# Kernel optimization log

Hardware: AMD Instinct MI355X
Metric: run time of the kernel (lower is better)

## Reference

```python
import jax, jax.numpy as jnp
import numpy as np

NUM_GRAPHS = 512  # number of segments (graphs) in the batch
N_NODES = 200000
HIDDEN = 256


def setup_inputs() -> dict:
    key = jax.random.key(0)
    ks = jax.random.split(key, 8)
    x = jax.random.normal(ks[0], (N_NODES, HIDDEN), dtype=jnp.float32)
    batch = jnp.sort(jax.random.randint(ks[1], (N_NODES,), 0, NUM_GRAPHS, dtype=jnp.int32))
    h4 = HIDDEN // 4
    w1 = jax.random.normal(ks[2], (HIDDEN, h4), dtype=jnp.float32) * (1.0 / np.sqrt(HIDDEN))
    b1 = jnp.zeros((h4,), dtype=jnp.float32)
    w2 = jax.random.normal(ks[3], (h4, 1), dtype=jnp.float32) * (1.0 / np.sqrt(h4))
    b2 = jnp.zeros((1,), dtype=jnp.float32)
    wp = jax.random.normal(ks[4], (3 * HIDDEN, HIDDEN), dtype=jnp.float32) * (1.0 / np.sqrt(3 * HIDDEN))
    bp = jnp.zeros((HIDDEN,), dtype=jnp.float32)
    gamma = jnp.ones((HIDDEN,), dtype=jnp.float32)
    beta = jnp.zeros((HIDDEN,), dtype=jnp.float32)
    return {"x": x, "batch": batch, "w1": w1, "b1": b1, "w2": w2, "b2": b2,
            "wp": wp, "bp": bp, "gamma": gamma, "beta": beta}


def reference(x, batch, w1, b1, w2, b2, wp, bp, gamma, beta):
    G = NUM_GRAPHS
    # --- global mean pool ---
    seg_sum = jax.ops.segment_sum(x, batch, num_segments=G)  # [G, H]
    counts = jax.ops.segment_sum(jnp.ones((x.shape[0],), x.dtype), batch, num_segments=G)
    z_mean = seg_sum / jnp.maximum(counts, 1.0)[:, None]
    # --- global max pool ---
    z_max = jax.ops.segment_max(x, batch, num_segments=G)
    z_max = jnp.where(jnp.isfinite(z_max), z_max, 0.0)  # guard empty segments
    # --- global attention pool (PyG GlobalAttention) ---
    gate = jnp.maximum(x @ w1 + b1, 0.0) @ w2 + b2  # [N, 1]
    g = gate[:, 0]
    g_max = jax.ops.segment_max(g, batch, num_segments=G)
    g_max = jnp.where(jnp.isfinite(g_max), g_max, 0.0)
    e = jnp.exp(g - g_max[batch])
    denom = jax.ops.segment_sum(e, batch, num_segments=G)
    w = e / jnp.maximum(denom, 1e-16)[batch]  # scatter-softmax weights [N]
    z_attn = jax.ops.segment_sum(w[:, None] * x, batch, num_segments=G)
    # --- concat + proj + layernorm ---
    z = jnp.concatenate([z_mean, z_max, z_attn], axis=-1)  # [G, 3H]
    y = z @ wp + bp  # [G, H]
    mu = jnp.mean(y, axis=-1, keepdims=True)
    var = jnp.mean(jnp.square(y - mu), axis=-1, keepdims=True)
    yhat = (y - mu) * jax.lax.rsqrt(var + 1e-5)
    return yhat * gamma + beta
```

## Files before the change

kernel.cpp:

```cpp
#include <hip/hip_runtime.h>
#include <math.h>

#define N_NODES 200000
#define NGRAPH  512
#define HID     256

typedef __attribute__((ext_vector_type(8))) short s16x8;
typedef __attribute__((ext_vector_type(4))) float f32x4;

__device__ __forceinline__ unsigned short f2bf_rne(float f) {
  unsigned int u = __float_as_uint(f);
  return (unsigned short)((u + 0x7fffu + ((u >> 16) & 1u)) >> 16);
}
__device__ __forceinline__ unsigned int pack2_bf16_rne(float a, float b) {
  unsigned int ua = __float_as_uint(a), ub = __float_as_uint(b);
  unsigned int ra = (ua + 0x7fffu + ((ua >> 16) & 1u)) >> 16;
  unsigned int rb = (ub + 0x7fffu + ((ub >> 16) & 1u)) & 0xffff0000u;
  return ra | rb;
}

__global__ __launch_bounds__(256, 2) void pool_partial(
    const float* __restrict__ x, const int* __restrict__ batch,
    const float* __restrict__ w1, const float* __restrict__ b1,
    const float* __restrict__ w2, const float* __restrict__ b2,
    float* __restrict__ pbuf)
{
  __shared__ __align__(16) short w1T[64 * 264];
  __shared__ int sb[2];
  __shared__ float sm[4], sd[4];

  const int tid = threadIdx.x;
  const int w = tid >> 6, lane = tid & 63, q = lane >> 4, c = lane & 15;
  const int seg = blockIdx.x >> 1, p = blockIdx.x & 1;

  if (tid < 2) {
    int target = seg + tid;
    int lo = 0, hi = N_NODES;
    while (lo < hi) { int mid = (lo + hi) >> 1; if (batch[mid] < target) lo = mid + 1; else hi = mid; }
    sb[tid] = lo;
  }
  for (int i = tid; i < 256 * 64; i += 256) {
    int k = i >> 6, n = i & 63;
    w1T[n * 264 + k] = (short)f2bf_rne(w1[i]);
  }
  __syncthreads();

  const int s0 = sb[0], e0 = sb[1];
  const int len = e0 - s0;
  const int ps = s0 + ((len * p) >> 1);
  const int pe = s0 + ((len * (p + 1)) >> 1);
  const int plen = pe - ps;

  float b1v[4], w2v[4];
#pragma unroll
  for (int nt = 0; nt < 4; ++nt) { b1v[nt] = b1[nt * 16 + c]; w2v[nt] = w2[nt * 16 + c]; }
  const float b2v = b2[0];

  f32x4 sum = (f32x4){0.f, 0.f, 0.f, 0.f};
  f32x4 mx  = (f32x4){-INFINITY, -INFINITY, -INFINITY, -INFINITY};
  f32x4 at  = (f32x4){0.f, 0.f, 0.f, 0.f};
  float den = 0.f, m = -INFINITY;

  const int ntiles = (plen + 15) >> 4;
  for (int t = w; t < ntiles; t += 4) {
    const int r0 = ps + (t << 4);
    const int lim = min(16, pe - r0);

    const int rowA = r0 + (c < lim ? c : 0);
    const float* ap = x + (size_t)rowA * HID + q * 8;
    union { s16x8 v; unsigned int u[4]; } ah[8];
#pragma unroll
    for (int half = 0; half < 2; ++half) {
      float4 t0[4], t1[4];
#pragma unroll
      for (int kk = 0; kk < 4; ++kk) {
        int kt = half * 4 + kk;
        t0[kk] = *(const float4*)(ap + kt * 32);
        t1[kk] = *(const float4*)(ap + kt * 32 + 4);
      }
#pragma unroll
      for (int kk = 0; kk < 4; ++kk) {
        int kt = half * 4 + kk;
        ah[kt].u[0] = pack2_bf16_rne(t0[kk].x, t0[kk].y);
        ah[kt].u[1] = pack2_bf16_rne(t0[kk].z, t0[kk].w);
        ah[kt].u[2] = pack2_bf16_rne(t1[kk].x, t1[kk].y);
        ah[kt].u[3] = pack2_bf16_rne(t1[kk].z, t1[kk].w);
      }
    }

    f32x4 acc[4];
#pragma unroll
    for (int nt = 0; nt < 4; ++nt) acc[nt] = (f32x4){0.f, 0.f, 0.f, 0.f};
#pragma unroll
    for (int kt = 0; kt < 8; ++kt) {
#pragma unroll
      for (int nt = 0; nt < 4; ++nt) {
        s16x8 bh = *(const s16x8*)&w1T[(nt * 16 + c) * 264 + kt * 32 + q * 8];
        acc[nt] = __builtin_amdgcn_mfma_f32_16x16x32_bf16(ah[kt].v, bh, acc[nt], 0, 0, 0);
      }
    }

    float gr[4];
#pragma unroll
    for (int r = 0; r < 4; ++r) {
      float sv = 0.f;
#pragma unroll
      for (int nt = 0; nt < 4; ++nt) {
        float h = acc[nt][r] + b1v[nt];
        h = h > 0.f ? h : 0.f;
        sv += h * w2v[nt];
      }
      sv += __shfl_xor(sv, 1, 64);
      sv += __shfl_xor(sv, 2, 64);
      sv += __shfl_xor(sv, 4, 64);
      sv += __shfl_xor(sv, 8, 64);
      gr[r] = sv + b2v;
    }

    float gm = -INFINITY;
#pragma unroll
    for (int r = 0; r < 4; ++r)
      gm = fmaxf(gm, (4 * q + r < lim) ? gr[r] : -INFINITY);
    gm = fmaxf(gm, __shfl_xor(gm, 16, 64));
    gm = fmaxf(gm, __shfl_xor(gm, 32, 64));

    float m_new = fmaxf(m, gm);
    float alpha = (m == -INFINITY) ? 0.f : __expf(m - m_new);
    at = at * alpha;
    den *= alpha;
    m = m_new;

#pragma unroll
    for (int i = 0; i < 16; ++i) {
      if (i < lim) {
        float gv = __shfl(gr[i & 3], (i >> 2) << 4, 64);
        float4 v = *(const float4*)(x + (size_t)(r0 + i) * HID + lane * 4);
        float ei = __expf(gv - m_new);
        den += ei;
        f32x4 f = (f32x4){v.x, v.y, v.z, v.w};
        sum = sum + f;
        mx[0] = fmaxf(mx[0], f[0]); mx[1] = fmaxf(mx[1], f[1]);
        mx[2] = fmaxf(mx[2], f[2]); mx[3] = fmaxf(mx[3], f[3]);
        at[0] = fmaf(ei, f[0], at[0]); at[1] = fmaf(ei, f[1], at[1]);
        at[2] = fmaf(ei, f[2], at[2]); at[3] = fmaf(ei, f[3], at[3]);
      }
    }
  }

  __syncthreads();
  float* scr = (float*)w1T;
  {
    float* p0 = scr + (w * 3 + 0) * 256;
    float* p1 = scr + (w * 3 + 1) * 256;
    float* p2 = scr + (w * 3 + 2) * 256;
    int f = lane * 4;
#pragma unroll
    for (int j = 0; j < 4; ++j) { p0[f + j] = sum[j]; p1[f + j] = mx[j]; p2[f + j] = at[j]; }
    if (lane == 0) { sm[w] = m; sd[w] = den; }
  }
  __syncthreads();
  {
    int f = tid;
    float M = fmaxf(fmaxf(sm[0], sm[1]), fmaxf(sm[2], sm[3]));
    float S = 0.f, MX = -INFINITY, A = 0.f, D = 0.f;
#pragma unroll
    for (int ww = 0; ww < 4; ++ww) {
      float sc = (sm[ww] == -INFINITY) ? 0.f : __expf(sm[ww] - M);
      S += scr[(ww * 3 + 0) * 256 + f];
      MX = fmaxf(MX, scr[(ww * 3 + 1) * 256 + f]);
      A = fmaf(sc, scr[(ww * 3 + 2) * 256 + f], A);
      D = fmaf(sc, sd[ww], D);
    }
    float* pr = pbuf + (size_t)blockIdx.x * 772;
    pr[f] = S; pr[256 + f] = MX; pr[512 + f] = A;
    if (tid == 0) { pr[768] = M; pr[769] = D; pr[770] = (float)plen; }
  }
}

__global__ __launch_bounds__(256) void pool_merge(
    const float* __restrict__ pbuf, float* __restrict__ zbuf)
{
  const int seg = blockIdx.x;
  const int f = threadIdx.x;
  const float* pa = pbuf + (size_t)(seg * 2) * 772;
  const float* pb = pa + 772;
  float m0 = pa[768], d0 = pa[769], c0 = pa[770];
  float m1 = pb[768], d1 = pb[769], c1 = pb[770];
  float M = fmaxf(m0, m1);
  float sc0 = (m0 == -INFINITY) ? 0.f : __expf(m0 - M);
  float sc1 = (m1 == -INFINITY) ? 0.f : __expf(m1 - M);
  float D = sc0 * d0 + sc1 * d1;
  float cnt = c0 + c1;
  float S  = pa[f] + pb[f];
  float MX = fmaxf(pa[256 + f], pb[256 + f]);
  float A  = sc0 * pa[512 + f] + sc1 * pb[512 + f];
  float* zr = zbuf + (size_t)seg * 768;
  zr[f]       = (cnt > 0.f) ? S / cnt : 0.f;
  zr[256 + f] = (cnt > 0.f) ? MX : 0.f;
  zr[512 + f] = (cnt > 0.f) ? A / fmaxf(D, 1e-16f) : 0.f;
}

__global__ __launch_bounds__(256) void head_ln(
    const float* __restrict__ zbuf, const float* __restrict__ wp,
    const float* __restrict__ bp, const float* __restrict__ gam,
    const float* __restrict__ bet, float* __restrict__ out)
{
  const int g = blockIdx.x;
  const int tid = threadIdx.x;
  const int w = tid >> 6, lane = tid & 63;
  __shared__ float z[768];
  __shared__ __align__(16) float part[4][256];
  __shared__ float red[256];

  for (int i = tid; i < 768; i += 256) z[i] = zbuf[(size_t)g * 768 + i];
  __syncthreads();

  f32x4 acc = (f32x4){0.f, 0.f, 0.f, 0.f};
  const float4* wp4 = (const float4*)wp;
  const int k0 = w * 192;
#pragma unroll 8
  for (int k = k0; k < k0 + 192; ++k) {
    float4 wv = wp4[(size_t)k * 64 + lane];
    float zk = z[k];
    acc[0] = fmaf(zk, wv.x, acc[0]);
    acc[1] = fmaf(zk, wv.y, acc[1]);
    acc[2] = fmaf(zk, wv.z, acc[2]);
    acc[3] = fmaf(zk, wv.w, acc[3]);
  }
  *(f32x4*)&part[w][lane * 4] = acc;
  __syncthreads();

  const int t = tid;
  float y = bp[t] + part[0][t] + part[1][t] + part[2][t] + part[3][t];

  red[t] = y;
  __syncthreads();
  for (int wd = 128; wd > 0; wd >>= 1) {
    if (t < wd) red[t] += red[t + wd];
    __syncthreads();
  }
  const float mu = red[0] * (1.f / 256.f);
  __syncthreads();
  float d = y - mu;
  red[t] = d * d;
  __syncthreads();
  for (int wd = 128; wd > 0; wd >>= 1) {
    if (t < wd) red[t] += red[t + wd];
    __syncthreads();
  }
  const float var = red[0] * (1.f / 256.f);
  const float is = rsqrtf(var + 1e-5f);
  out[(size_t)g * 256 + t] = fmaf(d * is, gam[t], bet[t]);
}

extern "C" void kernel_launch(void* const* d_in, const int* in_sizes, int n_in,
                              void* d_out, int out_size, void* d_ws, size_t ws_size,
                              hipStream_t stream) {
  const float* x   = (const float*)d_in[0];
  const int*   bat = (const int*)d_in[1];
  const float* w1  = (const float*)d_in[2];
  const float* b1  = (const float*)d_in[3];
  const float* w2  = (const float*)d_in[4];
  const float* b2  = (const float*)d_in[5];
  const float* wp  = (const float*)d_in[6];
  const float* bp  = (const float*)d_in[7];
  const float* gam = (const float*)d_in[8];
  const float* bet = (const float*)d_in[9];
  float* out = (float*)d_out;

  float* pbuf = (float*)d_ws;
  float* zbuf = (float*)((char*)d_ws + (size_t)1024 * 772 * 4);

  hipLaunchKernelGGL(pool_partial, dim3(NGRAPH * 2), dim3(256), 0, stream,
                     x, bat, w1, b1, w2, b2, pbuf);
  hipLaunchKernelGGL(pool_merge, dim3(NGRAPH), dim3(256), 0, stream, pbuf, zbuf);
  hipLaunchKernelGGL(head_ln, dim3(NGRAPH), dim3(256), 0, stream,
                     zbuf, wp, bp, gam, bet, out);
}
```

Baseline: 356.5 us.

## Split fused pooling into gate GEMM, segment softmax, and streaming pool passes

Replaces the single fused segment kernel, which computed the gate MLP and an online-softmax pool together, with separate stages. First a node-parallel gate kernel writes per-node scores, then a per-segment softmax kernel turns them into normalized weights, then a 4-way-split pool kernel streams x once more to accumulate sum, max and weighted sum. The aim is to decouple the MFMA gate work from segment boundaries for better load balance and to simplify the pooling inner loop. The cost is that x is read twice from memory instead of once, plus two extra launches.

```diff
diff --git a/kernel.cpp b/kernel.cpp
--- a/kernel.cpp
+++ b/kernel.cpp
@@ -4,6 +4,8 @@
 #define N_NODES 200000
 #define NGRAPH  512
 #define HID     256
+#define NTILES  (N_NODES / 16)
+#define PARTS   4
 
 typedef __attribute__((ext_vector_type(8))) short s16x8;
 typedef __attribute__((ext_vector_type(4))) float f32x4;
@@ -18,56 +20,39 @@
   unsigned int rb = (ub + 0x7fffu + ((ub >> 16) & 1u)) & 0xffff0000u;
   return ra | rb;
 }
-
-__global__ __launch_bounds__(256, 2) void pool_partial(
-    const float* __restrict__ x, const int* __restrict__ batch,
-    const float* __restrict__ w1, const float* __restrict__ b1,
-    const float* __restrict__ w2, const float* __restrict__ b2,
-    float* __restrict__ pbuf)
+__device__ __forceinline__ int lower_bound_batch(const int* __restrict__ batch, int target) {
+  int lo = 0, hi = N_NODES;
+  while (lo < hi) { int mid = (lo + hi) >> 1; if (batch[mid] < target) lo = mid + 1; else hi = mid; }
+  return lo;
+}
+__device__ __forceinline__ f32x4 vmax4(f32x4 a, f32x4 b) {
+  return (f32x4){fmaxf(a[0], b[0]), fmaxf(a[1], b[1]), fmaxf(a[2], b[2]), fmaxf(a[3], b[3])};
+}
+
+__global__ __launch_bounds__(256, 2) void gate_kernel(
+    const float* __restrict__ x, const float* __restrict__ w1,
+    const float* __restrict__ b1, const float* __restrict__ w2,
+    const float* __restrict__ b2, float* __restrict__ g)
 {
   __shared__ __align__(16) short w1T[64 * 264];
-  __shared__ int sb[2];
-  __shared__ float sm[4], sd[4];
-
   const int tid = threadIdx.x;
   const int w = tid >> 6, lane = tid & 63, q = lane >> 4, c = lane & 15;
-  const int seg = blockIdx.x >> 1, p = blockIdx.x & 1;
-
-  if (tid < 2) {
-    int target = seg + tid;
-    int lo = 0, hi = N_NODES;
-    while (lo < hi) { int mid = (lo + hi) >> 1; if (batch[mid] < target) lo = mid + 1; else hi = mid; }
-    sb[tid] = lo;
-  }
+
   for (int i = tid; i < 256 * 64; i += 256) {
     int k = i >> 6, n = i & 63;
     w1T[n * 264 + k] = (short)f2bf_rne(w1[i]);
   }
   __syncthreads();
 
-  const int s0 = sb[0], e0 = sb[1];
-  const int len = e0 - s0;
-  const int ps = s0 + ((len * p) >> 1);
-  const int pe = s0 + ((len * (p + 1)) >> 1);
-  const int plen = pe - ps;
-
   float b1v[4], w2v[4];
 #pragma unroll
   for (int nt = 0; nt < 4; ++nt) { b1v[nt] = b1[nt * 16 + c]; w2v[nt] = w2[nt * 16 + c]; }
   const float b2v = b2[0];
 
-  f32x4 sum = (f32x4){0.f, 0.f, 0.f, 0.f};
-  f32x4 mx  = (f32x4){-INFINITY, -INFINITY, -INFINITY, -INFINITY};
-  f32x4 at  = (f32x4){0.f, 0.f, 0.f, 0.f};
-  float den = 0.f, m = -INFINITY;
-
-  const int ntiles = (plen + 15) >> 4;
-  for (int t = w; t < ntiles; t += 4) {
-    const int r0 = ps + (t << 4);
-    const int lim = min(16, pe - r0);
-
-    const int rowA = r0 + (c < lim ? c : 0);
-    const float* ap = x + (size_t)rowA * HID + q * 8;
+  const int tstride = gridDim.x << 2;
+  for (int t = (blockIdx.x << 2) + w; t < NTILES; t += tstride) {
+    const int r0 = t << 4;
+    const float* ap = x + (size_t)(r0 + c) * HID + q * 8;
     union { s16x8 v; unsigned int u[4]; } ah[8];
 #pragma unroll
     for (int half = 0; half < 2; ++half) {
@@ -116,88 +101,139 @@
       sv += __shfl_xor(sv, 8, 64);
       gr[r] = sv + b2v;
     }
-
-    float gm = -INFINITY;
-#pragma unroll
-    for (int r = 0; r < 4; ++r)
-      gm = fmaxf(gm, (4 * q + r < lim) ? gr[r] : -INFINITY);
-    gm = fmaxf(gm, __shfl_xor(gm, 16, 64));
-    gm = fmaxf(gm, __shfl_xor(gm, 32, 64));
-
-    float m_new = fmaxf(m, gm);
-    float alpha = (m == -INFINITY) ? 0.f : __expf(m - m_new);
-    at = at * alpha;
-    den *= alpha;
-    m = m_new;
-
-#pragma unroll
-    for (int i = 0; i < 16; ++i) {
-      if (i < lim) {
-        float gv = __shfl(gr[i & 3], (i >> 2) << 4, 64);
-        float4 v = *(const float4*)(x + (size_t)(r0 + i) * HID + lane * 4);
-        float ei = __expf(gv - m_new);
-        den += ei;
-        f32x4 f = (f32x4){v.x, v.y, v.z, v.w};
-        sum = sum + f;
-        mx[0] = fmaxf(mx[0], f[0]); mx[1] = fmaxf(mx[1], f[1]);
-        mx[2] = fmaxf(mx[2], f[2]); mx[3] = fmaxf(mx[3], f[3]);
-        at[0] = fmaf(ei, f[0], at[0]); at[1] = fmaf(ei, f[1], at[1]);
-        at[2] = fmaf(ei, f[2], at[2]); at[3] = fmaf(ei, f[3], at[3]);
-      }
-    }
-  }
-
-  __syncthreads();
-  float* scr = (float*)w1T;
+    if (c == 0) {
+      float4 o = make_float4(gr[0], gr[1], gr[2], gr[3]);
+      *(float4*)(g + r0 + q * 4) = o;
+    }
+  }
+}
+
+__global__ __launch_bounds__(256) void seg_softmax(
+    const float* __restrict__ g, const int* __restrict__ batch,
+    float* __restrict__ wgt)
+{
+  __shared__ int sb[2];
+  __shared__ float red[4];
+  const int tid = threadIdx.x;
+  const int w = tid >> 6, lane = tid & 63;
+  if (tid < 2) sb[tid] = lower_bound_batch(batch, (int)blockIdx.x + tid);
+  __syncthreads();
+  const int s0 = sb[0], e0 = sb[1];
+
+  float m = -INFINITY;
+  for (int i = s0 + tid; i < e0; i += 256) m = fmaxf(m, g[i]);
+#pragma unroll
+  for (int off = 32; off > 0; off >>= 1) m = fmaxf(m, __shfl_xor(m, off, 64));
+  if (lane == 0) red[w] = m;
+  __syncthreads();
+  m = fmaxf(fmaxf(red[0], red[1]), fmaxf(red[2], red[3]));
+  __syncthreads();
+
+  float den = 0.f;
+  for (int i = s0 + tid; i < e0; i += 256) den += __expf(g[i] - m);
+#pragma unroll
+  for (int off = 32; off > 0; off >>= 1) den += __shfl_xor(den, off, 64);
+  if (lane == 0) red[w] = den;
+  __syncthreads();
+  den = red[0] + red[1] + red[2] + red[3];
+
+  const float inv = 1.f / fmaxf(den, 1e-16f);
+  for (int i = s0 + tid; i < e0; i += 256) wgt[i] = __expf(g[i] - m) * inv;
+}
+
+__global__ __launch_bounds__(256, 8) void pool_pass(
+    const float* __restrict__ x, const int* __restrict__ batch,
+    const float* __restrict__ wgt, float* __restrict__ pbuf)
+{
+  __shared__ int sb[2];
+  __shared__ __align__(16) float scr[12 * 256];
+  const int tid = threadIdx.x;
+  const int w = tid >> 6, lane = tid & 63;
+  const int seg = blockIdx.x >> 2, p = blockIdx.x & 3;
+
+  if (tid < 2) sb[tid] = lower_bound_batch(batch, seg + tid);
+  __syncthreads();
+  const int s0 = sb[0], len = sb[1] - s0;
+  const int ps = s0 + ((len * p) >> 2);
+  const int pe = s0 + ((len * (p + 1)) >> 2);
+
+  f32x4 sum = (f32x4){0.f, 0.f, 0.f, 0.f};
+  f32x4 at  = (f32x4){0.f, 0.f, 0.f, 0.f};
+  f32x4 mx  = (f32x4){-INFINITY, -INFINITY, -INFINITY, -INFINITY};
+
+  const float* xp = x + lane * 4;
+  int r = ps + w;
+  for (; r + 12 < pe; r += 16) {
+    float4 v0 = *(const float4*)(xp + (size_t)(r     ) * HID);
+    float4 v1 = *(const float4*)(xp + (size_t)(r +  4) * HID);
+    float4 v2 = *(const float4*)(xp + (size_t)(r +  8) * HID);
+    float4 v3 = *(const float4*)(xp + (size_t)(r + 12) * HID);
+    float w0 = wgt[r], w1v = wgt[r + 4], w2v = wgt[r + 8], w3v = wgt[r + 12];
+    f32x4 f0 = (f32x4){v0.x, v0.y, v0.z, v0.w};
+    f32x4 f1 = (f32x4){v1.x, v1.y, v1.z, v1.w};
+    f32x4 f2 = (f32x4){v2.x, v2.y, v2.z, v2.w};
+    f32x4 f3 = (f32x4){v3.x, v3.y, v3.z, v3.w};
+    sum = sum + ((f0 + f1) + (f2 + f3));
+    mx = vmax4(mx, vmax4(vmax4(f0, f1), vmax4(f2, f3)));
+#pragma unroll
+    for (int j = 0; j < 4; ++j) {
+      float a = fmaf(w0, f0[j], at[j]);
+      a = fmaf(w1v, f1[j], a);
+      a = fmaf(w2v, f2[j], a);
+      at[j] = fmaf(w3v, f3[j], a);
+    }
+  }
+  for (; r < pe; r += 4) {
+    float4 v = *(const float4*)(xp + (size_t)r * HID);
+    float wr = wgt[r];
+    f32x4 f = (f32x4){v.x, v.y, v.z, v.w};
+    sum = sum + f;
+    mx = vmax4(mx, f);
+#pragma unroll
+    for (int j = 0; j < 4; ++j) at[j] = fmaf(wr, f[j], at[j]);
+  }
+
   {
     float* p0 = scr + (w * 3 + 0) * 256;
     float* p1 = scr + (w * 3 + 1) * 256;
     float* p2 = scr + (w * 3 + 2) * 256;
-    int f = lane * 4;
-#pragma unroll
-    for (int j = 0; j < 4; ++j) { p0[f + j] = sum[j]; p1[f + j] = mx[j]; p2[f + j] = at[j]; }
-    if (lane == 0) { sm[w] = m; sd[w] = den; }
+    *(f32x4*)&p0[lane * 4] = sum;
+    *(f32x4*)&p1[lane * 4] = mx;
+    *(f32x4*)&p2[lane * 4] = at;
   }
   __syncthreads();
   {
-    int f = tid;
-    float M = fmaxf(fmaxf(sm[0], sm[1]), fmaxf(sm[2], sm[3]));
-    float S = 0.f, MX = -INFINITY, A = 0.f, D = 0.f;
+    const int f = tid;
+    float S = 0.f, MX = -INFINITY, A = 0.f;
 #pragma unroll
     for (int ww = 0; ww < 4; ++ww) {
-      float sc = (sm[ww] == -INFINITY) ? 0.f : __expf(sm[ww] - M);
       S += scr[(ww * 3 + 0) * 256 + f];
       MX = fmaxf(MX, scr[(ww * 3 + 1) * 256 + f]);
-      A = fmaf(sc, scr[(ww * 3 + 2) * 256 + f], A);
-      D = fmaf(sc, sd[ww], D);
+      A += scr[(ww * 3 + 2) * 256 + f];
     }
     float* pr = pbuf + (size_t)blockIdx.x * 772;
     pr[f] = S; pr[256 + f] = MX; pr[512 + f] = A;
-    if (tid == 0) { pr[768] = M; pr[769] = D; pr[770] = (float)plen; }
-  }
-}
-
-__global__ __launch_bounds__(256) void pool_merge(
+    if (tid == 0) pr[768] = (float)(pe - ps);
+  }
+}
+
+__global__ __launch_bounds__(256) void pool_merge2(
     const float* __restrict__ pbuf, float* __restrict__ zbuf)
 {
-  const int seg = blockIdx.x;
-  const int f = threadIdx.x;
-  const float* pa = pbuf + (size_t)(seg * 2) * 772;
-  const float* pb = pa + 772;
-  float m0 = pa[768], d0 = pa[769], c0 = pa[770];
-  float m1 = pb[768], d1 = pb[769], c1 = pb[770];
-  float M = fmaxf(m0, m1);
-  float sc0 = (m0 == -INFINITY) ? 0.f : __expf(m0 - M);
-  float sc1 = (m1 == -INFINITY) ? 0.f : __expf(m1 - M);
-  float D = sc0 * d0 + sc1 * d1;
-  float cnt = c0 + c1;
-  float S  = pa[f] + pb[f];
-  float MX = fmaxf(pa[256 + f], pb[256 + f]);
-  float A  = sc0 * pa[512 + f] + sc1 * pb[512 + f];
+  const int seg = blockIdx.x, f = threadIdx.x;
+  float S = 0.f, A = 0.f, MX = -INFINITY, cnt = 0.f;
+#pragma unroll
+  for (int pp = 0; pp < PARTS; ++pp) {
+    const float* pr = pbuf + (size_t)(seg * PARTS + pp) * 772;
+    S += pr[f];
+    MX = fmaxf(MX, pr[256 + f]);
+    A += pr[512 + f];
+    cnt += pr[768];
+  }
   float* zr = zbuf + (size_t)seg * 768;
-  zr[f]       = (cnt > 0.f) ? S / cnt : 0.f;
+  zr[f]       = S / fmaxf(cnt, 1.f);
   zr[256 + f] = (cnt > 0.f) ? MX : 0.f;
-  zr[512 + f] = (cnt > 0.f) ? A / fmaxf(D, 1e-16f) : 0.f;
+  zr[512 + f] = A;
 }
 
 __global__ __launch_bounds__(256) void head_ln(
@@ -268,12 +304,18 @@
   const float* bet = (const float*)d_in[9];
   float* out = (float*)d_out;
 
-  float* pbuf = (float*)d_ws;
-  float* zbuf = (float*)((char*)d_ws + (size_t)1024 * 772 * 4);
-
-  hipLaunchKernelGGL(pool_partial, dim3(NGRAPH * 2), dim3(256), 0, stream,
-                     x, bat, w1, b1, w2, b2, pbuf);
-  hipLaunchKernelGGL(pool_merge, dim3(NGRAPH), dim3(256), 0, stream, pbuf, zbuf);
+  float* gbuf = (float*)d_ws;
+  float* wgt  = gbuf + N_NODES;
+  float* pbuf = wgt + N_NODES;
+  float* zbuf = pbuf + (size_t)NGRAPH * PARTS * 772;
+
+  hipLaunchKernelGGL(gate_kernel, dim3(1024), dim3(256), 0, stream,
+                     x, w1, b1, w2, b2, gbuf);
+  hipLaunchKernelGGL(seg_softmax, dim3(NGRAPH), dim3(256), 0, stream,
+                     gbuf, bat, wgt);
+  hipLaunchKernelGGL(pool_pass, dim3(NGRAPH * PARTS), dim3(256), 0, stream,
+                     x, bat, wgt, pbuf);
+  hipLaunchKernelGGL(pool_merge2, dim3(NGRAPH), dim3(256), 0, stream, pbuf, zbuf);
   hipLaunchKernelGGL(head_ln, dim3(NGRAPH), dim3(256), 0, stream,
                      zbuf, wp, bp, gam, bet, out);
 }
```

Result: slower. 367.9 us (+3.2%).

## Fuse gate and pooling into one persistent node-tiled kernel with atomics

Applied to the files above, without the earlier changes.

Replaces the per-segment two-block partial plus merge scheme with a single kernel. It splits all node tiles evenly across 1024 waves, stages x rows into LDS with double-buffered global_load_lds, and keeps the bf16 w1 fragments in registers. Each wave accumulates per-segment sum, max, attention numerator and denominator, flushing them to global memory with atomics (max uses an order-preserving uint key) when the segment changes. The segment-max shift in the softmax is dropped in favour of a raw exp, which removes the running-max rescaling but risks overflow for large gate values and makes the float atomics order-nondeterministic. It also removes the merge kernel, adds a memset, and moves the count computation into the head kernel.

```diff
diff --git a/kernel.cpp b/kernel.cpp
--- a/kernel.cpp
+++ b/kernel.cpp
@@ -4,88 +4,131 @@
 #define N_NODES 200000
 #define NGRAPH  512
 #define HID     256
+#define NTILES  (N_NODES / 16)
+#define NBLK    256
+#define NWAVE   (NBLK * 4)
+#define TPW     (NTILES / NWAVE)
+#define TREM    (NTILES - NWAVE * TPW)
 
 typedef __attribute__((ext_vector_type(8))) short s16x8;
 typedef __attribute__((ext_vector_type(4))) float f32x4;
 
-__device__ __forceinline__ unsigned short f2bf_rne(float f) {
-  unsigned int u = __float_as_uint(f);
-  return (unsigned short)((u + 0x7fffu + ((u >> 16) & 1u)) >> 16);
-}
 __device__ __forceinline__ unsigned int pack2_bf16_rne(float a, float b) {
   unsigned int ua = __float_as_uint(a), ub = __float_as_uint(b);
   unsigned int ra = (ua + 0x7fffu + ((ua >> 16) & 1u)) >> 16;
   unsigned int rb = (ub + 0x7fffu + ((ub >> 16) & 1u)) & 0xffff0000u;
   return ra | rb;
 }
-
-__global__ __launch_bounds__(256, 2) void pool_partial(
+__device__ __forceinline__ int lower_bound_batch(const int* __restrict__ batch, int target) {
+  int lo = 0, hi = N_NODES;
+  while (lo < hi) { int mid = (lo + hi) >> 1; if (batch[mid] < target) lo = mid + 1; else hi = mid; }
+  return lo;
+}
+__device__ __forceinline__ unsigned fkey(float f) {
+  unsigned u = __float_as_uint(f);
+  return (u >> 31) ? ~u : (u | 0x80000000u);
+}
+
+__global__ __launch_bounds__(256, 1) void fused_gate_pool(
     const float* __restrict__ x, const int* __restrict__ batch,
     const float* __restrict__ w1, const float* __restrict__ b1,
     const float* __restrict__ w2, const float* __restrict__ b2,
-    float* __restrict__ pbuf)
+    float* __restrict__ gsum, unsigned* __restrict__ gmx,
+    float* __restrict__ gat, float* __restrict__ gden)
 {
-  __shared__ __align__(16) short w1T[64 * 264];
-  __shared__ int sb[2];
-  __shared__ float sm[4], sd[4];
+  struct Buf { float xrow[16][256]; int bat[64]; };
+  __shared__ __align__(16) Buf stg[4][2];
 
   const int tid = threadIdx.x;
   const int w = tid >> 6, lane = tid & 63, q = lane >> 4, c = lane & 15;
-  const int seg = blockIdx.x >> 1, p = blockIdx.x & 1;
-
-  if (tid < 2) {
-    int target = seg + tid;
-    int lo = 0, hi = N_NODES;
-    while (lo < hi) { int mid = (lo + hi) >> 1; if (batch[mid] < target) lo = mid + 1; else hi = mid; }
-    sb[tid] = lo;
-  }
-  for (int i = tid; i < 256 * 64; i += 256) {
-    int k = i >> 6, n = i & 63;
-    w1T[n * 264 + k] = (short)f2bf_rne(w1[i]);
-  }
-  __syncthreads();
-
-  const int s0 = sb[0], e0 = sb[1];
-  const int len = e0 - s0;
-  const int ps = s0 + ((len * p) >> 1);
-  const int pe = s0 + ((len * (p + 1)) >> 1);
-  const int plen = pe - ps;
-
+  const int gw = blockIdx.x * 4 + w;
+
+  const int t0   = gw * TPW + (gw < TREM ? gw : TREM);
+  const int tend = t0 + TPW + (gw < TREM ? 1 : 0);
+
+  s16x8 bh[4][8];
+#pragma unroll
+  for (int nt = 0; nt < 4; ++nt) {
+#pragma unroll
+    for (int kt = 0; kt < 8; ++kt) {
+      float f[8];
+#pragma unroll
+      for (int j = 0; j < 8; ++j)
+        f[j] = w1[(size_t)(kt * 32 + q * 8 + j) * 64 + nt * 16 + c];
+      union { s16x8 v; unsigned u[4]; } tmp;
+      tmp.u[0] = pack2_bf16_rne(f[0], f[1]);
+      tmp.u[1] = pack2_bf16_rne(f[2], f[3]);
+      tmp.u[2] = pack2_bf16_rne(f[4], f[5]);
+      tmp.u[3] = pack2_bf16_rne(f[6], f[7]);
+      bh[nt][kt] = tmp.v;
+    }
+  }
   float b1v[4], w2v[4];
 #pragma unroll
   for (int nt = 0; nt < 4; ++nt) { b1v[nt] = b1[nt * 16 + c]; w2v[nt] = w2[nt * 16 + c]; }
   const float b2v = b2[0];
 
+  int soff[8];
+#pragma unroll
+  for (int s = 0; s < 8; ++s) soff[s] = (lane * 16) ^ (s << 4);
+  const int csw = (c & 7) << 4;
+
   f32x4 sum = (f32x4){0.f, 0.f, 0.f, 0.f};
+  f32x4 at  = (f32x4){0.f, 0.f, 0.f, 0.f};
   f32x4 mx  = (f32x4){-INFINITY, -INFINITY, -INFINITY, -INFINITY};
-  f32x4 at  = (f32x4){0.f, 0.f, 0.f, 0.f};
-  float den = 0.f, m = -INFINITY;
-
-  const int ntiles = (plen + 15) >> 4;
-  for (int t = w; t < ntiles; t += 4) {
-    const int r0 = ps + (t << 4);
-    const int lim = min(16, pe - r0);
-
-    const int rowA = r0 + (c < lim ? c : 0);
-    const float* ap = x + (size_t)rowA * HID + q * 8;
-    union { s16x8 v; unsigned int u[4]; } ah[8];
-#pragma unroll
-    for (int half = 0; half < 2; ++half) {
-      float4 t0[4], t1[4];
-#pragma unroll
-      for (int kk = 0; kk < 4; ++kk) {
-        int kt = half * 4 + kk;
-        t0[kk] = *(const float4*)(ap + kt * 32);
-        t1[kk] = *(const float4*)(ap + kt * 32 + 4);
-      }
-#pragma unroll
-      for (int kk = 0; kk < 4; ++kk) {
-        int kt = half * 4 + kk;
-        ah[kt].u[0] = pack2_bf16_rne(t0[kk].x, t0[kk].y);
-        ah[kt].u[1] = pack2_bf16_rne(t0[kk].z, t0[kk].w);
-        ah[kt].u[2] = pack2_bf16_rne(t1[kk].x, t1[kk].y);
-        ah[kt].u[3] = pack2_bf16_rne(t1[kk].z, t1[kk].w);
-      }
+  float den = 0.f;
+  int curseg = -1;
+
+  auto STAGE = [&](int t, int b) {
+    const char* rowbase = (const char*)x + (size_t)t * 16384;
+#pragma unroll
+    for (int r = 0; r < 16; ++r) {
+      const void* gp = rowbase + r * 1024 + soff[r & 7];
+      __builtin_amdgcn_global_load_lds(
+          (const __attribute__((address_space(1))) void*)gp,
+          (__attribute__((address_space(3))) void*)&stg[w][b].xrow[r][0],
+          16, 0, 0);
+    }
+    const void* bp2 = (const void*)(batch + t * 16 + (lane & 15));
+    __builtin_amdgcn_global_load_lds(
+        (const __attribute__((address_space(1))) void*)bp2,
+        (__attribute__((address_space(3))) void*)&stg[w][b].bat[0],
+        4, 0, 0);
+  };
+
+  auto FLUSH = [&](int seg) {
+    float* sp = gsum + (size_t)seg * 256 + lane * 4;
+    float* ap = gat  + (size_t)seg * 256 + lane * 4;
+    unsigned* mp = gmx + (size_t)seg * 256 + lane * 4;
+#pragma unroll
+    for (int j = 0; j < 4; ++j) {
+      atomicAdd(&sp[j], sum[j]);
+      atomicAdd(&ap[j], at[j]);
+      atomicMax(&mp[j], fkey(mx[j]));
+    }
+    if (lane == 0) atomicAdd(&gden[seg], den);
+  };
+
+  STAGE(t0, 0);
+  STAGE(t0 + 1, 1);
+
+  for (int t = t0; t < tend; ++t) {
+    const int b = (t - t0) & 1;
+    if (t + 1 < tend) { asm volatile("s_waitcnt vmcnt(17)" ::: "memory"); }
+    else              { asm volatile("s_waitcnt vmcnt(0)"  ::: "memory"); }
+    __builtin_amdgcn_sched_barrier(0);
+
+    const char* rb = (const char*)&stg[w][b].xrow[c][0];
+    union { s16x8 v; unsigned u[4]; } ah[8];
+#pragma unroll
+    for (int kt = 0; kt < 8; ++kt) {
+      const int base = kt * 128 + q * 32;
+      float4 t0v = *(const float4*)(rb + ((base)      ^ csw));
+      float4 t1v = *(const float4*)(rb + ((base + 16) ^ csw));
+      ah[kt].u[0] = pack2_bf16_rne(t0v.x, t0v.y);
+      ah[kt].u[1] = pack2_bf16_rne(t0v.z, t0v.w);
+      ah[kt].u[2] = pack2_bf16_rne(t1v.x, t1v.y);
+      ah[kt].u[3] = pack2_bf16_rne(t1v.z, t1v.w);
     }
 
     f32x4 acc[4];
@@ -94,13 +137,11 @@
 #pragma unroll
     for (int kt = 0; kt < 8; ++kt) {
 #pragma unroll
-      for (int nt = 0; nt < 4; ++nt) {
-        s16x8 bh = *(const s16x8*)&w1T[(nt * 16 + c) * 264 + kt * 32 + q * 8];
-        acc[nt] = __builtin_amdgcn_mfma_f32_16x16x32_bf16(ah[kt].v, bh, acc[nt], 0, 0, 0);
-      }
-    }
-
-    float gr[4];
+      for (int nt = 0; nt < 4; ++nt)
+        acc[nt] = __builtin_amdgcn_mfma_f32_16x16x32_bf16(ah[kt].v, bh[nt][kt], acc[nt], 0, 0, 0);
+    }
+
+    float er[4];
 #pragma unroll
     for (int r = 0; r < 4; ++r) {
       float sv = 0.f;
@@ -114,105 +155,65 @@
       sv += __shfl_xor(sv, 2, 64);
       sv += __shfl_xor(sv, 4, 64);
       sv += __shfl_xor(sv, 8, 64);
-      gr[r] = sv + b2v;
-    }
-
-    float gm = -INFINITY;
-#pragma unroll
-    for (int r = 0; r < 4; ++r)
-      gm = fmaxf(gm, (4 * q + r < lim) ? gr[r] : -INFINITY);
-    gm = fmaxf(gm, __shfl_xor(gm, 16, 64));
-    gm = fmaxf(gm, __shfl_xor(gm, 32, 64));
-
-    float m_new = fmaxf(m, gm);
-    float alpha = (m == -INFINITY) ? 0.f : __expf(m - m_new);
-    at = at * alpha;
-    den *= alpha;
-    m = m_new;
+      er[r] = __expf(sv + b2v);
+    }
 
 #pragma unroll
     for (int i = 0; i < 16; ++i) {
-      if (i < lim) {
-        float gv = __shfl(gr[i & 3], (i >> 2) << 4, 64);
-        float4 v = *(const float4*)(x + (size_t)(r0 + i) * HID + lane * 4);
-        float ei = __expf(gv - m_new);
-        den += ei;
-        f32x4 f = (f32x4){v.x, v.y, v.z, v.w};
-        sum = sum + f;
-        mx[0] = fmaxf(mx[0], f[0]); mx[1] = fmaxf(mx[1], f[1]);
-        mx[2] = fmaxf(mx[2], f[2]); mx[3] = fmaxf(mx[3], f[3]);
-        at[0] = fmaf(ei, f[0], at[0]); at[1] = fmaf(ei, f[1], at[1]);
-        at[2] = fmaf(ei, f[2], at[2]); at[3] = fmaf(ei, f[3], at[3]);
+      int sg = __builtin_amdgcn_readfirstlane(stg[w][b].bat[i]);
+      if (sg != curseg) {
+        if (curseg >= 0) FLUSH(curseg);
+        sum = (f32x4){0.f, 0.f, 0.f, 0.f};
+        at  = (f32x4){0.f, 0.f, 0.f, 0.f};
+        mx  = (f32x4){-INFINITY, -INFINITY, -INFINITY, -INFINITY};
+        den = 0.f;
+        curseg = sg;
       }
-    }
-  }
-
-  __syncthreads();
-  float* scr = (float*)w1T;
-  {
-    float* p0 = scr + (w * 3 + 0) * 256;
-    float* p1 = scr + (w * 3 + 1) * 256;
-    float* p2 = scr + (w * 3 + 2) * 256;
-    int f = lane * 4;
-#pragma unroll
-    for (int j = 0; j < 4; ++j) { p0[f + j] = sum[j]; p1[f + j] = mx[j]; p2[f + j] = at[j]; }
-    if (lane == 0) { sm[w] = m; sd[w] = den; }
-  }
-  __syncthreads();
-  {
-    int f = tid;
-    float M = fmaxf(fmaxf(sm[0], sm[1]), fmaxf(sm[2], sm[3]));
-    float S = 0.f, MX = -INFINITY, A = 0.f, D = 0.f;
-#pragma unroll
-    for (int ww = 0; ww < 4; ++ww) {
-      float sc = (sm[ww] == -INFINITY) ? 0.f : __expf(sm[ww] - M);
-      S += scr[(ww * 3 + 0) * 256 + f];
-      MX = fmaxf(MX, scr[(ww * 3 + 1) * 256 + f]);
-      A = fmaf(sc, scr[(ww * 3 + 2) * 256 + f], A);
-      D = fmaf(sc, sd[ww], D);
-    }
-    float* pr = pbuf + (size_t)blockIdx.x * 772;
-    pr[f] = S; pr[256 + f] = MX; pr[512 + f] = A;
-    if (tid == 0) { pr[768] = M; pr[769] = D; pr[770] = (float)plen; }
-  }
-}
-
-__global__ __launch_bounds__(256) void pool_merge(
-    const float* __restrict__ pbuf, float* __restrict__ zbuf)
-{
-  const int seg = blockIdx.x;
-  const int f = threadIdx.x;
-  const float* pa = pbuf + (size_t)(seg * 2) * 772;
-  const float* pb = pa + 772;
-  float m0 = pa[768], d0 = pa[769], c0 = pa[770];
-  float m1 = pb[768], d1 = pb[769], c1 = pb[770];
-  float M = fmaxf(m0, m1);
-  float sc0 = (m0 == -INFINITY) ? 0.f : __expf(m0 - M);
-  float sc1 = (m1 == -INFINITY) ? 0.f : __expf(m1 - M);
-  float D = sc0 * d0 + sc1 * d1;
-  float cnt = c0 + c1;
-  float S  = pa[f] + pb[f];
-  float MX = fmaxf(pa[256 + f], pb[256 + f]);
-  float A  = sc0 * pa[512 + f] + sc1 * pb[512 + f];
-  float* zr = zbuf + (size_t)seg * 768;
-  zr[f]       = (cnt > 0.f) ? S / cnt : 0.f;
-  zr[256 + f] = (cnt > 0.f) ? MX : 0.f;
-  zr[512 + f] = (cnt > 0.f) ? A / fmaxf(D, 1e-16f) : 0.f;
+      float ei = __shfl(er[i & 3], (i >> 2) << 4, 64);
+      const float4 v = *(const float4*)((const char*)&stg[w][b].xrow[i][0] +
+                                        ((lane * 16) ^ ((i & 7) << 4)));
+      den += ei;
+      sum[0] += v.x; sum[1] += v.y; sum[2] += v.z; sum[3] += v.w;
+      mx[0] = fmaxf(mx[0], v.x); mx[1] = fmaxf(mx[1], v.y);
+      mx[2] = fmaxf(mx[2], v.z); mx[3] = fmaxf(mx[3], v.w);
+      at[0] = fmaf(ei, v.x, at[0]); at[1] = fmaf(ei, v.y, at[1]);
+      at[2] = fmaf(ei, v.z, at[2]); at[3] = fmaf(ei, v.w, at[3]);
+    }
+
+    if (t + 2 < tend) STAGE(t + 2, b);
+  }
+  if (curseg >= 0) FLUSH(curseg);
 }
 
 __global__ __launch_bounds__(256) void head_ln(
-    const float* __restrict__ zbuf, const float* __restrict__ wp,
+    const float* __restrict__ gsum, const unsigned* __restrict__ gmx,
+    const float* __restrict__ gat, const float* __restrict__ gden,
+    const int* __restrict__ batch, const float* __restrict__ wp,
     const float* __restrict__ bp, const float* __restrict__ gam,
     const float* __restrict__ bet, float* __restrict__ out)
 {
   const int g = blockIdx.x;
   const int tid = threadIdx.x;
   const int w = tid >> 6, lane = tid & 63;
+  __shared__ int sb[2];
   __shared__ float z[768];
   __shared__ __align__(16) float part[4][256];
   __shared__ float red[256];
 
-  for (int i = tid; i < 768; i += 256) z[i] = zbuf[(size_t)g * 768 + i];
+  if (tid < 2) sb[tid] = lower_bound_batch(batch, g + tid);
+  __syncthreads();
+  const float cnt = (float)(sb[1] - sb[0]);
+
+  {
+    const float s = gsum[(size_t)g * 256 + tid];
+    const unsigned k = gmx[(size_t)g * 256 + tid];
+    const unsigned u = (k & 0x80000000u) ? (k ^ 0x80000000u) : ~k;
+    const float a = gat[(size_t)g * 256 + tid];
+    const float den = gden[g];
+    z[tid]       = (cnt > 0.f) ? s / cnt : 0.f;
+    z[256 + tid] = (cnt > 0.f) ? __uint_as_float(u) : 0.f;
+    z[512 + tid] = a / fmaxf(den, 1e-16f);
+  }
   __syncthreads();
 
   f32x4 acc = (f32x4){0.f, 0.f, 0.f, 0.f};
@@ -268,12 +269,15 @@
   const float* bet = (const float*)d_in[9];
   float* out = (float*)d_out;
 
-  float* pbuf = (float*)d_ws;
-  float* zbuf = (float*)((char*)d_ws + (size_t)1024 * 772 * 4);
-
-  hipLaunchKernelGGL(pool_partial, dim3(NGRAPH * 2), dim3(256), 0, stream,
-                     x, bat, w1, b1, w2, b2, pbuf);
-  hipLaunchKernelGGL(pool_merge, dim3(NGRAPH), dim3(256), 0, stream, pbuf, zbuf);
+  float* gsum   = (float*)d_ws;
+  unsigned* gmx = (unsigned*)(gsum + (size_t)NGRAPH * 256);
+  float* gat    = (float*)(gmx + (size_t)NGRAPH * 256);
+  float* gden   = gat + (size_t)NGRAPH * 256;
+  const size_t zbytes = ((size_t)NGRAPH * 256 * 3 + NGRAPH) * 4;
+
+  hipMemsetAsync(d_ws, 0, zbytes, stream);
+  hipLaunchKernelGGL(fused_gate_pool, dim3(NBLK), dim3(256), 0, stream,
+                     x, bat, w1, b1, w2, b2, gsum, gmx, gat, gden);
   hipLaunchKernelGGL(head_ln, dim3(NGRAPH), dim3(256), 0, stream,
-                     zbuf, wp, bp, gam, bet, out);
-}
+                     gsum, gmx, gat, gden, bat, wp, bp, gam, bet, out);
+}
```

After: 339.7 us. 4.7% less time.
